# Kernel tuning notes

Measured on AMD Instinct MI355X. Metric: run time of the kernel, lower is better.

The kernel has to match this reference:

```python
import jax, jax.numpy as jnp
import numpy as np

C_Z = 128
N_HEADS = 4
HEAD_DIM = 32
TOTAL = N_HEADS * HEAD_DIM
B, N = 1, 256


def setup_inputs() -> dict:
    key = jax.random.key(0)
    ks = jax.random.split(key, 10)
    s = lambda k, sh: jax.random.normal(k, sh, dtype=jnp.float32) * 0.02
    return {
        "pair_representation": jax.random.normal(ks[0], (B, N, N, C_Z), dtype=jnp.float32),
        "ln_gamma": jnp.ones((C_Z,), jnp.float32),
        "ln_beta": jnp.zeros((C_Z,), jnp.float32),
        "Wq": s(ks[1], (C_Z, TOTAL)),
        "Wk": s(ks[2], (C_Z, TOTAL)),
        "Wv": s(ks[3], (C_Z, TOTAL)),
        "Wb": s(ks[4], (C_Z, N_HEADS)),
        "Wg": s(ks[5], (C_Z, TOTAL)),
        "bg": jnp.zeros((TOTAL,), jnp.float32),
        "Wo": s(ks[6], (TOTAL, C_Z)),
        "bo": jnp.zeros((C_Z,), jnp.float32),
    }


def reference(pair_representation, ln_gamma, ln_beta, Wq, Wk, Wv, Wb, Wg, bg, Wo, bo):
    x = pair_representation
    # LayerNorm over c_z
    mu = jnp.mean(x, axis=-1, keepdims=True)
    var = jnp.mean((x - mu) ** 2, axis=-1, keepdims=True)
    x = (x - mu) * jax.lax.rsqrt(var + 1e-5) * ln_gamma + ln_beta

    b, n, _, _ = x.shape
    split = lambda t: t.reshape(b, n, n, N_HEADS, HEAD_DIM)
    Q = split(x @ Wq)  # [b,i,j,h,d]
    K = split(x @ Wk)
    V = split(x @ Wv)
    G = jax.nn.sigmoid(split(x @ Wg + bg))
    Bias = x @ Wb  # [b,j,k,h]

    scores = jnp.einsum("bijhd,bikhd->bijkh", Q, K) / np.float32(np.sqrt(HEAD_DIM))
    scores = scores + Bias[:, None]  # broadcast over i
    attn = jax.nn.softmax(scores, axis=3)  # over k
    vals = jnp.einsum("bijkh,bikhd->bijhd", attn, V)
    vals = (G * vals).reshape(b, n, n, TOTAL)
    return vals @ Wo + bo
```

## Files before the change

### kernel.cpp

```cpp
#include <hip/hip_runtime.h>
#include <hip/hip_bf16.h>


#define QSCALE 0.17677669529663687f

typedef __attribute__((ext_vector_type(8))) short bf16x8;
typedef __attribute__((ext_vector_type(4))) float f32x4;

__device__ __forceinline__ ushort f2bf(float f) {
    uint32_t u = __builtin_bit_cast(uint32_t, f);
    uint32_t r = (u + 0x7FFFu + ((u >> 16) & 1u)) >> 16;
    return (ushort)r;
}
__device__ __forceinline__ float bf2f(ushort b) {
    return __builtin_bit_cast(float, ((uint32_t)b) << 16);
}
__device__ __forceinline__ uint pk2(float a, float b) {
    union { __hip_bfloat162 h; uint u; } cv;
    cv.h = __float22bfloat162_rn(make_float2(a, b));
    return cv.u;
}
__device__ __forceinline__ float4 ld4f(const float* p) { return *(const float4*)p; }

__global__ __launch_bounds__(256) void prep_kernel(
    const float* __restrict__ Wq, const float* __restrict__ Wk, const float* __restrict__ Wv,
    const float* __restrict__ Wb, const float* __restrict__ Wg, const float* __restrict__ Wo,
    ushort* __restrict__ Wfrag, ushort* __restrict__ WoFrag)
{
    int idx = blockIdx.x * 256 + threadIdx.x;
    if (idx < 67584) {
        int j = idx & 7, lane = (idx >> 3) & 63, ks = (idx >> 9) & 3, ct = idx >> 11;
        int n = ct * 16 + (lane & 15);
        int k = ks * 32 + (lane >> 4) * 8 + j;
        float v = 0.f;
        if (n < 128)      v = Wq[k * 128 + n] * QSCALE;
        else if (n < 256) v = Wk[k * 128 + (n - 128)];
        else if (n < 384) v = Wv[k * 128 + (n - 256)];
        else if (n < 512) v = Wg[k * 128 + (n - 384)];
        else if (n < 516) v = Wb[k * 4 + (n - 512)];
        Wfrag[idx] = f2bf(v);
    } else {
        int idx2 = idx - 67584;
        int j = idx2 & 7, lane = (idx2 >> 3) & 63, ks = (idx2 >> 9) & 3, ct = idx2 >> 11;
        int n = ct * 16 + (lane & 15);
        int k = ks * 32 + (lane >> 4) * 8 + j;
        WoFrag[idx2] = f2bf(Wo[k * 128 + n]);
    }
}

__global__ __launch_bounds__(256) void proj_kernel(
    const float* __restrict__ x, const float* __restrict__ gamma, const float* __restrict__ beta,
    const ushort* __restrict__ Wfrag, const float* __restrict__ bg,
    ushort* __restrict__ Qg, ushort* __restrict__ Kg, ushort* __restrict__ Vtg,
    ushort* __restrict__ Gg, float* __restrict__ BbF)
{
    __shared__ ushort Bs[11 * 2048];
    const int t = threadIdx.x;
    const int wave = t >> 6, lane = t & 63, m = lane & 15, quad = lane >> 4;
    const int p0 = blockIdx.x * 64;
    const int arow = p0 + wave * 16 + m;

    float4 xa[4][2];
    float sum = 0.f, ssq = 0.f;
#pragma unroll
    for (int ks = 0; ks < 4; ++ks) {
        const float* rp = x + arow * 128 + ks * 32 + quad * 8;
        xa[ks][0] = ld4f(rp);
        xa[ks][1] = ld4f(rp + 4);
#pragma unroll
        for (int q4 = 0; q4 < 2; ++q4) {
            float4 v = xa[ks][q4];
            sum += v.x + v.y + v.z + v.w;
            ssq += v.x * v.x + v.y * v.y + v.z * v.z + v.w * v.w;
        }
    }
    sum += __shfl_xor(sum, 16); ssq += __shfl_xor(ssq, 16);
    sum += __shfl_xor(sum, 32); ssq += __shfl_xor(ssq, 32);
    const float mu   = sum * (1.f / 128.f);
    const float var  = ssq * (1.f / 128.f) - mu * mu;
    const float rstd = rsqrtf(var + 1e-5f);

    bf16x8 xf[4];
#pragma unroll
    for (int ks = 0; ks < 4; ++ks) {
        union { bf16x8 v; uint u[4]; } xu;
#pragma unroll
        for (int q4 = 0; q4 < 2; ++q4) {
            const int c = ks * 32 + quad * 8 + q4 * 4;
            float4 g4 = ld4f(gamma + c);
            float4 b4 = ld4f(beta + c);
            float4 v = xa[ks][q4];
            float n0 = (v.x - mu) * rstd * g4.x + b4.x;
            float n1 = (v.y - mu) * rstd * g4.y + b4.y;
            float n2 = (v.z - mu) * rstd * g4.z + b4.z;
            float n3 = (v.w - mu) * rstd * g4.w + b4.w;
            xu.u[q4 * 2]     = pk2(n0, n1);
            xu.u[q4 * 2 + 1] = pk2(n2, n3);
        }
        xf[ks] = xu.v;
    }

    const int p = arow;
    const int i = p >> 8, j2 = p & 255;

    for (int phase = 0; phase < 3; ++phase) {
        const int ctbase = phase * 11;
        __syncthreads();
        const uint4* src = (const uint4*)(Wfrag + ctbase * 2048);
        uint4* dst = (uint4*)Bs;
#pragma unroll
        for (int r = 0; r < 11; ++r) dst[r * 256 + t] = src[r * 256 + t];
        __syncthreads();

        for (int ctl = 0; ctl < 11; ++ctl) {
            const int ct = ctbase + ctl;
            f32x4 acc = (f32x4){0.f, 0.f, 0.f, 0.f};
#pragma unroll
            for (int ks = 0; ks < 4; ++ks) {
                bf16x8 wfr = ((const bf16x8*)Bs)[(ctl * 4 + ks) * 64 + lane];
                acc = __builtin_amdgcn_mfma_f32_16x16x32_bf16(wfr, xf[ks], acc, 0, 0, 0);
            }
            if (ct < 32) {
                const int cls = ct >> 3;
                const int npb = (ct & 7) * 16 + quad * 4;
                const int hh = npb >> 5, d0 = npb & 31;
                if (cls == 2) {
                    const int vb = ((i * 4 + hh) * 32 + d0) * 256 + j2;
#pragma unroll
                    for (int r = 0; r < 4; ++r)
                        Vtg[vb + r * 256] = f2bf(acc[r]);
                } else {
                    const int off = ((i * 4 + hh) * 256 + j2) * 32 + d0;
                    uint2 u;
                    if (cls == 3) {
                        float4 bg4 = ld4f(&bg[npb]);
                        float z0 = 1.f / (1.f + __expf(-(acc[0] + bg4.x)));
                        float z1 = 1.f / (1.f + __expf(-(acc[1] + bg4.y)));
                        float z2 = 1.f / (1.f + __expf(-(acc[2] + bg4.z)));
                        float z3 = 1.f / (1.f + __expf(-(acc[3] + bg4.w)));
                        u.x = pk2(z0, z1); u.y = pk2(z2, z3);
                        *(uint2*)(&Gg[off]) = u;
                    } else {
                        u.x = pk2(acc[0], acc[1]); u.y = pk2(acc[2], acc[3]);
                        if (cls == 0) *(uint2*)(&Qg[off]) = u;
                        else          *(uint2*)(&Kg[off]) = u;
                    }
                }
            } else if (quad == 0) {
#pragma unroll
                for (int r = 0; r < 4; ++r) {
                    int addr = (((r * 16 + (i >> 4)) * 16 + (j2 >> 4)) * 64 +
                                ((j2 & 15) >> 2) * 16 + (i & 15)) * 4 + (j2 & 3);
                    BbF[addr] = acc[r];
                }
            }
        }
    }
}

__global__ __launch_bounds__(256) void attn_kernel(
    const ushort* __restrict__ Qg, const ushort* __restrict__ Kg, const ushort* __restrict__ Vtg,
    const ushort* __restrict__ Gg, const float* __restrict__ BbF, ushort* __restrict__ gvals)
{
    __shared__ ushort Pl[4][64 * 72];
    const int t = threadIdx.x;
    const int wave = t >> 6, lane = t & 63, m = lane & 15, quad = lane >> 4;
    const int ih = blockIdx.x, i = ih >> 2, h = ih & 3;

    const int j0 = wave * 64;
    bf16x8 qf[4];
#pragma unroll
    for (int jt = 0; jt < 4; ++jt)
        qf[jt] = *(const bf16x8*)(Qg + ih * 8192 + (j0 + jt * 16 + m) * 32 + quad * 8);

    f32x4 O[4][2];
    float lsum[4];
#pragma unroll
    for (int jt = 0; jt < 4; ++jt) {
        O[jt][0] = (f32x4){0.f, 0.f, 0.f, 0.f};
        O[jt][1] = (f32x4){0.f, 0.f, 0.f, 0.f};
        lsum[jt] = 0.f;
    }

    for (int kt2 = 0; kt2 < 4; ++kt2) {
        const int k0 = kt2 * 64;
        bf16x8 kf[4];
#pragma unroll
        for (int kk = 0; kk < 4; ++kk)
            kf[kk] = *(const bf16x8*)(Kg + ih * 8192 + (k0 + kk * 16 + m) * 32 + quad * 8);

#pragma unroll
        for (int jt = 0; jt < 4; ++jt) {
            const int jtg = wave * 4 + jt;
#pragma unroll
            for (int kk = 0; kk < 4; ++kk) {
                const int ktg = kt2 * 4 + kk;
                f32x4 bias = *(const f32x4*)(BbF + (((h * 16 + jtg) * 16 + ktg) * 64 + lane) * 4);
                f32x4 S = __builtin_amdgcn_mfma_f32_16x16x32_bf16(kf[kk], qf[jt], bias, 0, 0, 0);
                float pv0 = __expf(S[0]);
                float pv1 = __expf(S[1]);
                float pv2 = __expf(S[2]);
                float pv3 = __expf(S[3]);
                lsum[jt] += pv0 + pv1 + pv2 + pv3;
                uint2 u; u.x = pk2(pv0, pv1); u.y = pk2(pv2, pv3);
                *(uint2*)(&Pl[wave][(jt * 16 + m) * 72 + kk * 16 + quad * 4]) = u;
            }
        }
#pragma unroll
        for (int kc = 0; kc < 2; ++kc) {
            bf16x8 pf[4], vf[2];
#pragma unroll
            for (int jt = 0; jt < 4; ++jt)
                pf[jt] = *(const bf16x8*)(&Pl[wave][(jt * 16 + m) * 72 + kc * 32 + quad * 8]);
#pragma unroll
            for (int dt = 0; dt < 2; ++dt)
                vf[dt] = *(const bf16x8*)(Vtg + (ih * 32 + dt * 16 + m) * 256 + k0 + kc * 32 + quad * 8);
#pragma unroll
            for (int jt = 0; jt < 4; ++jt)
#pragma unroll
                for (int dt = 0; dt < 2; ++dt)
                    O[jt][dt] = __builtin_amdgcn_mfma_f32_16x16x32_bf16(
                        vf[dt], pf[jt], O[jt][dt], 0, 0, 0);
        }
    }

#pragma unroll
    for (int jt = 0; jt < 4; ++jt) {
        float s = lsum[jt];
        s += __shfl_xor(s, 16);
        s += __shfl_xor(s, 32);
        lsum[jt] = 1.f / s;
    }

#pragma unroll
    for (int jt = 0; jt < 4; ++jt) {
        const int j = j0 + jt * 16 + m;
        const float rl = lsum[jt];
#pragma unroll
        for (int dt = 0; dt < 2; ++dt) {
            const int d0 = dt * 16 + quad * 4;
            ushort4 gv = *(const ushort4*)(&Gg[ih * 8192 + j * 32 + d0]);
            float v0 = O[jt][dt][0] * rl * bf2f(gv.x);
            float v1 = O[jt][dt][1] * rl * bf2f(gv.y);
            float v2 = O[jt][dt][2] * rl * bf2f(gv.z);
            float v3 = O[jt][dt][3] * rl * bf2f(gv.w);
            uint2 u; u.x = pk2(v0, v1); u.y = pk2(v2, v3);
            *(uint2*)(&gvals[(i * 256 + j) * 128 + h * 32 + d0]) = u;
        }
    }
}

__global__ __launch_bounds__(256) void oproj_kernel(
    const ushort* __restrict__ gvals, const ushort* __restrict__ WoFrag,
    const float* __restrict__ bo, float* __restrict__ out)
{
    __shared__ ushort Bs[8 * 2048];
    const int t = threadIdx.x;
    const int wave = t >> 6, lane = t & 63, m = lane & 15, quad = lane >> 4;
    const int p0 = blockIdx.x * 64;
    {
        const uint4* src = (const uint4*)WoFrag;
        uint4* dst = (uint4*)Bs;
#pragma unroll
        for (int r = 0; r < 8; ++r) dst[r * 256 + t] = src[r * 256 + t];
    }
    bf16x8 gf[4];
    const int p = p0 + wave * 16 + m;
#pragma unroll
    for (int ks = 0; ks < 4; ++ks)
        gf[ks] = *(const bf16x8*)(gvals + p * 128 + ks * 32 + quad * 8);
    __syncthreads();

#pragma unroll
    for (int ct = 0; ct < 8; ++ct) {
        f32x4 acc = (f32x4){0.f, 0.f, 0.f, 0.f};
#pragma unroll
        for (int ks = 0; ks < 4; ++ks) {
            bf16x8 wfr = ((const bf16x8*)Bs)[(ct * 4 + ks) * 64 + lane];
            acc = __builtin_amdgcn_mfma_f32_16x16x32_bf16(wfr, gf[ks], acc, 0, 0, 0);
        }
        const int c0 = ct * 16 + quad * 4;
        float4 bov = ld4f(&bo[c0]);
        float4 v = make_float4(acc[0] + bov.x, acc[1] + bov.y,
                               acc[2] + bov.z, acc[3] + bov.w);
        *(float4*)(&out[p * 128 + c0]) = v;
    }
}

extern "C" void kernel_launch(void* const* d_in, const int* in_sizes, int n_in,
                              void* d_out, int out_size, void* d_ws, size_t ws_size,
                              hipStream_t stream) {
    const float* x     = (const float*)d_in[0];
    const float* gamma = (const float*)d_in[1];
    const float* beta  = (const float*)d_in[2];
    const float* Wq    = (const float*)d_in[3];
    const float* Wk    = (const float*)d_in[4];
    const float* Wv    = (const float*)d_in[5];
    const float* Wb    = (const float*)d_in[6];
    const float* Wg    = (const float*)d_in[7];
    const float* bg    = (const float*)d_in[8];
    const float* Wo    = (const float*)d_in[9];
    const float* bo    = (const float*)d_in[10];

    ushort* ws     = (ushort*)d_ws;
    ushort* Wfrag  = ws;
    ushort* WoFrag = Wfrag + 67584;
    ushort* Qg     = WoFrag + 16384;
    ushort* Kg     = Qg + 8388608;
    ushort* Vtg    = Kg + 8388608;
    ushort* Gg     = Vtg + 8388608;
    ushort* gvals  = Gg + 8388608;
    float*  BbF    = (float*)(gvals + 8388608);

    prep_kernel<<<328, 256, 0, stream>>>(Wq, Wk, Wv, Wb, Wg, Wo, Wfrag, WoFrag);
    proj_kernel<<<1024, 256, 0, stream>>>(x, gamma, beta, Wfrag, bg, Qg, Kg, Vtg, Gg, BbF);
    attn_kernel<<<1024, 256, 0, stream>>>(Qg, Kg, Vtg, Gg, BbF, gvals);
    oproj_kernel<<<1024, 256, 0, stream>>>(gvals, WoFrag, bo, (float*)d_out);
}
```

Baseline: 173.4 us.

## Fuse projection, attention and output projection into one per-row kernel

Replaces the separate projection, attention and output-projection kernels with a single fused kernel per row i. It keeps K, V, Q and the gated values in 160KB of LDS with XOR swizzling, which removes the global round-trips of the Q/K/V/gvals intermediates. The pair bias moves to its own LayerNorm+matvec kernel so it is ready before the fused pass. The cost is only 256 blocks of 512 threads with heavy LDS use, so occupancy is low and the gate values still pass through global memory.

```diff
diff --git a/kernel.cpp b/kernel.cpp
--- a/kernel.cpp
+++ b/kernel.cpp
@@ -20,27 +20,25 @@
     cv.h = __float22bfloat162_rn(make_float2(a, b));
     return cv.u;
 }
-__device__ __forceinline__ float4 ld4f(const float* p) { return *(const float4*)p; }
 
 __global__ __launch_bounds__(256) void prep_kernel(
     const float* __restrict__ Wq, const float* __restrict__ Wk, const float* __restrict__ Wv,
-    const float* __restrict__ Wb, const float* __restrict__ Wg, const float* __restrict__ Wo,
+    const float* __restrict__ Wg, const float* __restrict__ Wo,
     ushort* __restrict__ Wfrag, ushort* __restrict__ WoFrag)
 {
     int idx = blockIdx.x * 256 + threadIdx.x;
-    if (idx < 67584) {
+    if (idx < 65536) {
         int j = idx & 7, lane = (idx >> 3) & 63, ks = (idx >> 9) & 3, ct = idx >> 11;
         int n = ct * 16 + (lane & 15);
         int k = ks * 32 + (lane >> 4) * 8 + j;
-        float v = 0.f;
+        float v;
         if (n < 128)      v = Wq[k * 128 + n] * QSCALE;
         else if (n < 256) v = Wk[k * 128 + (n - 128)];
         else if (n < 384) v = Wv[k * 128 + (n - 256)];
-        else if (n < 512) v = Wg[k * 128 + (n - 384)];
-        else if (n < 516) v = Wb[k * 4 + (n - 512)];
+        else              v = Wg[k * 128 + (n - 384)];
         Wfrag[idx] = f2bf(v);
     } else {
-        int idx2 = idx - 67584;
+        int idx2 = idx - 65536;
         int j = idx2 & 7, lane = (idx2 >> 3) & 63, ks = (idx2 >> 9) & 3, ct = idx2 >> 11;
         int n = ct * 16 + (lane & 15);
         int k = ks * 32 + (lane >> 4) * 8 + j;
@@ -48,242 +46,371 @@
     }
 }
 
-__global__ __launch_bounds__(256) void proj_kernel(
+__global__ __launch_bounds__(256) void bias_kernel(
     const float* __restrict__ x, const float* __restrict__ gamma, const float* __restrict__ beta,
-    const ushort* __restrict__ Wfrag, const float* __restrict__ bg,
-    ushort* __restrict__ Qg, ushort* __restrict__ Kg, ushort* __restrict__ Vtg,
-    ushort* __restrict__ Gg, float* __restrict__ BbF)
+    const float* __restrict__ Wb, float* __restrict__ BbF)
 {
-    __shared__ ushort Bs[11 * 2048];
+    __shared__ float WbS[512];
+    __shared__ float gS[128];
+    __shared__ float bS[128];
     const int t = threadIdx.x;
+    if (t < 128)      { *(f32x4*)&WbS[t * 4] = *(const f32x4*)(Wb + t * 4); }
+    else if (t < 160) { int c = (t - 128) * 4; *(f32x4*)&gS[c] = *(const f32x4*)(gamma + c); }
+    else if (t < 192) { int c = (t - 160) * 4; *(f32x4*)&bS[c] = *(const f32x4*)(beta + c); }
+    __syncthreads();
+
     const int wave = t >> 6, lane = t & 63, m = lane & 15, quad = lane >> 4;
-    const int p0 = blockIdx.x * 64;
-    const int arow = p0 + wave * 16 + m;
-
-    float4 xa[4][2];
+    const int p = blockIdx.x * 64 + wave * 16 + m;
+
+    const float* rp0 = x + (size_t)p * 128;
+    f32x4 xa[4][2];
     float sum = 0.f, ssq = 0.f;
 #pragma unroll
     for (int ks = 0; ks < 4; ++ks) {
-        const float* rp = x + arow * 128 + ks * 32 + quad * 8;
-        xa[ks][0] = ld4f(rp);
-        xa[ks][1] = ld4f(rp + 4);
+        xa[ks][0] = *(const f32x4*)(rp0 + ks * 32 + quad * 8);
+        xa[ks][1] = *(const f32x4*)(rp0 + ks * 32 + quad * 8 + 4);
 #pragma unroll
         for (int q4 = 0; q4 < 2; ++q4) {
-            float4 v = xa[ks][q4];
-            sum += v.x + v.y + v.z + v.w;
-            ssq += v.x * v.x + v.y * v.y + v.z * v.z + v.w * v.w;
+            f32x4 v = xa[ks][q4];
+            sum += v[0] + v[1] + v[2] + v[3];
+            ssq += v[0]*v[0] + v[1]*v[1] + v[2]*v[2] + v[3]*v[3];
         }
     }
     sum += __shfl_xor(sum, 16); ssq += __shfl_xor(ssq, 16);
     sum += __shfl_xor(sum, 32); ssq += __shfl_xor(ssq, 32);
     const float mu   = sum * (1.f / 128.f);
-    const float var  = ssq * (1.f / 128.f) - mu * mu;
-    const float rstd = rsqrtf(var + 1e-5f);
-
-    bf16x8 xf[4];
+    const float rstd = rsqrtf(ssq * (1.f / 128.f) - mu * mu + 1e-5f);
+
+    float b0 = 0.f, b1 = 0.f, b2 = 0.f, b3 = 0.f;
 #pragma unroll
     for (int ks = 0; ks < 4; ++ks) {
-        union { bf16x8 v; uint u[4]; } xu;
 #pragma unroll
         for (int q4 = 0; q4 < 2; ++q4) {
             const int c = ks * 32 + quad * 8 + q4 * 4;
-            float4 g4 = ld4f(gamma + c);
-            float4 b4 = ld4f(beta + c);
-            float4 v = xa[ks][q4];
-            float n0 = (v.x - mu) * rstd * g4.x + b4.x;
-            float n1 = (v.y - mu) * rstd * g4.y + b4.y;
-            float n2 = (v.z - mu) * rstd * g4.z + b4.z;
-            float n3 = (v.w - mu) * rstd * g4.w + b4.w;
-            xu.u[q4 * 2]     = pk2(n0, n1);
-            xu.u[q4 * 2 + 1] = pk2(n2, n3);
-        }
-        xf[ks] = xu.v;
-    }
-
-    const int p = arow;
-    const int i = p >> 8, j2 = p & 255;
-
-    for (int phase = 0; phase < 3; ++phase) {
-        const int ctbase = phase * 11;
-        __syncthreads();
-        const uint4* src = (const uint4*)(Wfrag + ctbase * 2048);
-        uint4* dst = (uint4*)Bs;
-#pragma unroll
-        for (int r = 0; r < 11; ++r) dst[r * 256 + t] = src[r * 256 + t];
-        __syncthreads();
-
-        for (int ctl = 0; ctl < 11; ++ctl) {
-            const int ct = ctbase + ctl;
-            f32x4 acc = (f32x4){0.f, 0.f, 0.f, 0.f};
-#pragma unroll
-            for (int ks = 0; ks < 4; ++ks) {
-                bf16x8 wfr = ((const bf16x8*)Bs)[(ctl * 4 + ks) * 64 + lane];
-                acc = __builtin_amdgcn_mfma_f32_16x16x32_bf16(wfr, xf[ks], acc, 0, 0, 0);
-            }
-            if (ct < 32) {
-                const int cls = ct >> 3;
-                const int npb = (ct & 7) * 16 + quad * 4;
-                const int hh = npb >> 5, d0 = npb & 31;
-                if (cls == 2) {
-                    const int vb = ((i * 4 + hh) * 32 + d0) * 256 + j2;
-#pragma unroll
-                    for (int r = 0; r < 4; ++r)
-                        Vtg[vb + r * 256] = f2bf(acc[r]);
-                } else {
-                    const int off = ((i * 4 + hh) * 256 + j2) * 32 + d0;
-                    uint2 u;
-                    if (cls == 3) {
-                        float4 bg4 = ld4f(&bg[npb]);
-                        float z0 = 1.f / (1.f + __expf(-(acc[0] + bg4.x)));
-                        float z1 = 1.f / (1.f + __expf(-(acc[1] + bg4.y)));
-                        float z2 = 1.f / (1.f + __expf(-(acc[2] + bg4.z)));
-                        float z3 = 1.f / (1.f + __expf(-(acc[3] + bg4.w)));
-                        u.x = pk2(z0, z1); u.y = pk2(z2, z3);
-                        *(uint2*)(&Gg[off]) = u;
-                    } else {
-                        u.x = pk2(acc[0], acc[1]); u.y = pk2(acc[2], acc[3]);
-                        if (cls == 0) *(uint2*)(&Qg[off]) = u;
-                        else          *(uint2*)(&Kg[off]) = u;
-                    }
-                }
-            } else if (quad == 0) {
-#pragma unroll
-                for (int r = 0; r < 4; ++r) {
-                    int addr = (((r * 16 + (i >> 4)) * 16 + (j2 >> 4)) * 64 +
-                                ((j2 & 15) >> 2) * 16 + (i & 15)) * 4 + (j2 & 3);
-                    BbF[addr] = acc[r];
-                }
-            }
-        }
-    }
-}
-
-__global__ __launch_bounds__(256) void attn_kernel(
-    const ushort* __restrict__ Qg, const ushort* __restrict__ Kg, const ushort* __restrict__ Vtg,
-    const ushort* __restrict__ Gg, const float* __restrict__ BbF, ushort* __restrict__ gvals)
+            f32x4 v = xa[ks][q4];
+#pragma unroll
+            for (int e = 0; e < 4; ++e) {
+                float xn = (v[e] - mu) * rstd * gS[c + e] + bS[c + e];
+                f32x4 w = *(const f32x4*)&WbS[(c + e) * 4];
+                b0 += xn * w[0]; b1 += xn * w[1]; b2 += xn * w[2]; b3 += xn * w[3];
+            }
+        }
+    }
+    b0 += __shfl_xor(b0, 16); b1 += __shfl_xor(b1, 16); b2 += __shfl_xor(b2, 16); b3 += __shfl_xor(b3, 16);
+    b0 += __shfl_xor(b0, 32); b1 += __shfl_xor(b1, 32); b2 += __shfl_xor(b2, 32); b3 += __shfl_xor(b3, 32);
+
+    if (quad == 0) {
+        const int row = p >> 8, col = p & 255;
+        float bb[4] = {b0, b1, b2, b3};
+#pragma unroll
+        for (int r = 0; r < 4; ++r) {
+            int addr = (((r * 16 + (row >> 4)) * 16 + (col >> 4)) * 64 +
+                        ((col & 15) >> 2) * 16 + (row & 15)) * 4 + (col & 3);
+            BbF[addr] = bb[r];
+        }
+    }
+}
+
+__device__ __forceinline__ void stage32(ushort* dst, const ushort* src, int t) {
+    const uint4* s = (const uint4*)src;
+    uint4* d = (uint4*)dst;
+#pragma unroll
+    for (int c = 0; c < 4; ++c) d[c * 512 + t] = s[c * 512 + t];
+}
+
+__global__ __launch_bounds__(512, 2) void fused_kernel(
+    const float* __restrict__ x, const float* __restrict__ gamma, const float* __restrict__ beta,
+    const ushort* __restrict__ Wfrag, const ushort* __restrict__ WoFrag,
+    const float* __restrict__ bg, const float* __restrict__ bo,
+    const float* __restrict__ BbF, ushort* __restrict__ Gg, float* __restrict__ out)
 {
-    __shared__ ushort Pl[4][64 * 72];
+    extern __shared__ __align__(16) ushort smem[];
+    ushort* KL  = smem;
+    ushort* VL  = smem + 32768;
+    ushort* SCR = smem + 65536;
+
     const int t = threadIdx.x;
     const int wave = t >> 6, lane = t & 63, m = lane & 15, quad = lane >> 4;
-    const int ih = blockIdx.x, i = ih >> 2, h = ih & 3;
-
-    const int j0 = wave * 64;
-    bf16x8 qf[4];
-#pragma unroll
-    for (int jt = 0; jt < 4; ++jt)
-        qf[jt] = *(const bf16x8*)(Qg + ih * 8192 + (j0 + jt * 16 + m) * 32 + quad * 8);
-
-    f32x4 O[4][2];
-    float lsum[4];
-#pragma unroll
-    for (int jt = 0; jt < 4; ++jt) {
-        O[jt][0] = (f32x4){0.f, 0.f, 0.f, 0.f};
-        O[jt][1] = (f32x4){0.f, 0.f, 0.f, 0.f};
-        lsum[jt] = 0.f;
-    }
-
-    for (int kt2 = 0; kt2 < 4; ++kt2) {
-        const int k0 = kt2 * 64;
-        bf16x8 kf[4];
-#pragma unroll
-        for (int kk = 0; kk < 4; ++kk)
-            kf[kk] = *(const bf16x8*)(Kg + ih * 8192 + (k0 + kk * 16 + m) * 32 + quad * 8);
-
+    const int i = blockIdx.x;
+
+    bf16x8 xf[2][4];
+#pragma unroll
+    for (int grp = 0; grp < 2; ++grp) {
+        const int j = wave * 32 + grp * 16 + m;
+        const float* rp0 = x + (size_t)(i * 256 + j) * 128;
+        f32x4 xa[4][2];
+        float sum = 0.f, ssq = 0.f;
+#pragma unroll
+        for (int ks = 0; ks < 4; ++ks) {
+            xa[ks][0] = *(const f32x4*)(rp0 + ks * 32 + quad * 8);
+            xa[ks][1] = *(const f32x4*)(rp0 + ks * 32 + quad * 8 + 4);
+#pragma unroll
+            for (int q4 = 0; q4 < 2; ++q4) {
+                f32x4 v = xa[ks][q4];
+                sum += v[0] + v[1] + v[2] + v[3];
+                ssq += v[0]*v[0] + v[1]*v[1] + v[2]*v[2] + v[3]*v[3];
+            }
+        }
+        sum += __shfl_xor(sum, 16); ssq += __shfl_xor(ssq, 16);
+        sum += __shfl_xor(sum, 32); ssq += __shfl_xor(ssq, 32);
+        const float mu   = sum * (1.f / 128.f);
+        const float rstd = rsqrtf(ssq * (1.f / 128.f) - mu * mu + 1e-5f);
+#pragma unroll
+        for (int ks = 0; ks < 4; ++ks) {
+            union { bf16x8 v; uint u[4]; } xu;
+#pragma unroll
+            for (int q4 = 0; q4 < 2; ++q4) {
+                const int c = ks * 32 + quad * 8 + q4 * 4;
+                f32x4 g4 = *(const f32x4*)(gamma + c);
+                f32x4 b4 = *(const f32x4*)(beta + c);
+                f32x4 v = xa[ks][q4];
+                float n0 = (v[0] - mu) * rstd * g4[0] + b4[0];
+                float n1 = (v[1] - mu) * rstd * g4[1] + b4[1];
+                float n2 = (v[2] - mu) * rstd * g4[2] + b4[2];
+                float n3 = (v[3] - mu) * rstd * g4[3] + b4[3];
+                xu.u[q4 * 2]     = pk2(n0, n1);
+                xu.u[q4 * 2 + 1] = pk2(n2, n3);
+            }
+            xf[grp][ks] = xu.v;
+        }
+    }
+
+    stage32(SCR, Wfrag, t);
+    __syncthreads();
+#pragma unroll
+    for (int ct = 0; ct < 8; ++ct) {
+        bf16x8 wfr[4];
+#pragma unroll
+        for (int ks = 0; ks < 4; ++ks) wfr[ks] = ((const bf16x8*)SCR)[(ct * 4 + ks) * 64 + lane];
+#pragma unroll
+        for (int grp = 0; grp < 2; ++grp) {
+            f32x4 acc = (f32x4){0.f, 0.f, 0.f, 0.f};
+#pragma unroll
+            for (int ks = 0; ks < 4; ++ks)
+                acc = __builtin_amdgcn_mfma_f32_16x16x32_bf16(wfr[ks], xf[grp][ks], acc, 0, 0, 0);
+            const int pj = wave * 32 + grp * 16 + m;
+            const int c0 = ct * 16 + quad * 4;
+            const int idx = (pj * 128 + c0) ^ ((pj & 7) << 3);
+            uint2 u; u.x = pk2(acc[0], acc[1]); u.y = pk2(acc[2], acc[3]);
+            *(uint2*)(KL + idx) = u;
+        }
+    }
+    __syncthreads();
+
+    const int h = wave >> 1;
+    const int jb = (wave & 1) * 128;
+    bf16x8 qf[8];
+#pragma unroll
+    for (int jt8 = 0; jt8 < 8; ++jt8) {
+        const int j = jb + jt8 * 16 + m;
+        const int idx = (j * 128 + h * 32 + quad * 8) ^ ((j & 7) << 3);
+        qf[jt8] = *(const bf16x8*)(KL + idx);
+    }
+
+    stage32(SCR, Wfrag + 16384, t);
+    __syncthreads();
+#pragma unroll
+    for (int ct = 0; ct < 8; ++ct) {
+        bf16x8 wfr[4];
+#pragma unroll
+        for (int ks = 0; ks < 4; ++ks) wfr[ks] = ((const bf16x8*)SCR)[(ct * 4 + ks) * 64 + lane];
+        const int hk = ct >> 1;
+        const int d0 = (ct & 1) * 16 + quad * 4;
+#pragma unroll
+        for (int grp = 0; grp < 2; ++grp) {
+            f32x4 acc = (f32x4){0.f, 0.f, 0.f, 0.f};
+#pragma unroll
+            for (int ks = 0; ks < 4; ++ks)
+                acc = __builtin_amdgcn_mfma_f32_16x16x32_bf16(wfr[ks], xf[grp][ks], acc, 0, 0, 0);
+            const int k = wave * 32 + grp * 16 + m;
+            const int idx = (hk * 8192 + (k >> 1) * 64 + (k & 1) * 32 + d0) ^ (((k >> 1) & 7) << 3);
+            uint2 u; u.x = pk2(acc[0], acc[1]); u.y = pk2(acc[2], acc[3]);
+            *(uint2*)(KL + idx) = u;
+        }
+    }
+
+    __syncthreads();
+    stage32(SCR, Wfrag + 32768, t);
+    __syncthreads();
+#pragma unroll
+    for (int ct = 0; ct < 8; ++ct) {
+        bf16x8 wfr[4];
+#pragma unroll
+        for (int ks = 0; ks < 4; ++ks) wfr[ks] = ((const bf16x8*)SCR)[(ct * 4 + ks) * 64 + lane];
+        const int hv = ct >> 1;
+        const int d0 = (ct & 1) * 16 + quad * 4;
+#pragma unroll
+        for (int grp = 0; grp < 2; ++grp) {
+            f32x4 acc = (f32x4){0.f, 0.f, 0.f, 0.f};
+#pragma unroll
+            for (int ks = 0; ks < 4; ++ks)
+                acc = __builtin_amdgcn_mfma_f32_16x16x32_bf16(wfr[ks], xf[grp][ks], acc, 0, 0, 0);
+            const int k = wave * 32 + grp * 16 + m;
+#pragma unroll
+            for (int r = 0; r < 4; ++r) {
+                const int d = d0 + r;
+                const int idx = ((hv * 32 + d) * 256 + k) ^ ((d & 7) << 3);
+                VL[idx] = f2bf(acc[r]);
+            }
+        }
+    }
+
+    __syncthreads();
+    stage32(SCR, Wfrag + 49152, t);
+    __syncthreads();
+#pragma unroll
+    for (int ct = 0; ct < 8; ++ct) {
+        bf16x8 wfr[4];
+#pragma unroll
+        for (int ks = 0; ks < 4; ++ks) wfr[ks] = ((const bf16x8*)SCR)[(ct * 4 + ks) * 64 + lane];
+        const int c0 = ct * 16 + quad * 4;
+        f32x4 bg4 = *(const f32x4*)(bg + c0);
+#pragma unroll
+        for (int grp = 0; grp < 2; ++grp) {
+            f32x4 acc = (f32x4){0.f, 0.f, 0.f, 0.f};
+#pragma unroll
+            for (int ks = 0; ks < 4; ++ks)
+                acc = __builtin_amdgcn_mfma_f32_16x16x32_bf16(wfr[ks], xf[grp][ks], acc, 0, 0, 0);
+            float z0 = 1.f / (1.f + __expf(-(acc[0] + bg4[0])));
+            float z1 = 1.f / (1.f + __expf(-(acc[1] + bg4[1])));
+            float z2 = 1.f / (1.f + __expf(-(acc[2] + bg4[2])));
+            float z3 = 1.f / (1.f + __expf(-(acc[3] + bg4[3])));
+            uint2 u; u.x = pk2(z0, z1); u.y = pk2(z2, z3);
+            const int gidx = (((wave * 8 + ct) * 2 + grp) * 64 + lane) * 4;
+            *(uint2*)(Gg + (size_t)i * 32768 + gidx) = u;
+        }
+    }
+    __syncthreads();
+
+    ushort* Pw = SCR + wave * 2048;
+    f32x4 O[2][4][2];
+    float lsum[2][4];
+#pragma unroll
+    for (int u = 0; u < 2; ++u)
 #pragma unroll
         for (int jt = 0; jt < 4; ++jt) {
-            const int jtg = wave * 4 + jt;
-#pragma unroll
-            for (int kk = 0; kk < 4; ++kk) {
-                const int ktg = kt2 * 4 + kk;
-                f32x4 bias = *(const f32x4*)(BbF + (((h * 16 + jtg) * 16 + ktg) * 64 + lane) * 4);
-                f32x4 S = __builtin_amdgcn_mfma_f32_16x16x32_bf16(kf[kk], qf[jt], bias, 0, 0, 0);
-                float pv0 = __expf(S[0]);
-                float pv1 = __expf(S[1]);
-                float pv2 = __expf(S[2]);
-                float pv3 = __expf(S[3]);
-                lsum[jt] += pv0 + pv1 + pv2 + pv3;
-                uint2 u; u.x = pk2(pv0, pv1); u.y = pk2(pv2, pv3);
-                *(uint2*)(&Pl[wave][(jt * 16 + m) * 72 + kk * 16 + quad * 4]) = u;
-            }
-        }
-#pragma unroll
-        for (int kc = 0; kc < 2; ++kc) {
-            bf16x8 pf[4], vf[2];
+            O[u][jt][0] = (f32x4){0.f, 0.f, 0.f, 0.f};
+            O[u][jt][1] = (f32x4){0.f, 0.f, 0.f, 0.f};
+            lsum[u][jt] = 0.f;
+        }
+
+#pragma unroll
+    for (int u = 0; u < 2; ++u) {
+        const int jq = (wave & 1) * 2 + u;
+        for (int kh = 0; kh < 8; ++kh) {
+            const int k0 = kh * 32;
+            bf16x8 kf[2];
+#pragma unroll
+            for (int kk = 0; kk < 2; ++kk) {
+                const int k = k0 + kk * 16 + m;
+                const int idx = (h * 8192 + (k >> 1) * 64 + (k & 1) * 32 + quad * 8) ^ (((k >> 1) & 7) << 3);
+                kf[kk] = *(const bf16x8*)(KL + idx);
+            }
+#pragma unroll
+            for (int jt = 0; jt < 4; ++jt) {
+                const int jtg = jq * 4 + jt;
+#pragma unroll
+                for (int kk = 0; kk < 2; ++kk) {
+                    const int ktg = kh * 2 + kk;
+                    f32x4 S = *(const f32x4*)(BbF + (((h * 16 + jtg) * 16 + ktg) * 64 + lane) * 4);
+                    S = __builtin_amdgcn_mfma_f32_16x16x32_bf16(kf[kk], qf[u * 4 + jt], S, 0, 0, 0);
+                    float p0 = __expf(S[0]), p1 = __expf(S[1]);
+                    float p2 = __expf(S[2]), p3 = __expf(S[3]);
+                    lsum[u][jt] += p0 + p1 + p2 + p3;
+                    const int jl = jt * 16 + m;
+                    const int pidx = ((jl >> 1) * 64 + (jl & 1) * 32 + kk * 16 + quad * 4) ^ (((jl >> 1) & 7) << 3);
+                    uint2 up; up.x = pk2(p0, p1); up.y = pk2(p2, p3);
+                    *(uint2*)(Pw + pidx) = up;
+                }
+            }
+            bf16x8 vf[2], pf[4];
+#pragma unroll
+            for (int dt = 0; dt < 2; ++dt) {
+                const int d = dt * 16 + m;
+                const int idx = ((h * 32 + d) * 256 + k0 + quad * 8) ^ ((d & 7) << 3);
+                vf[dt] = *(const bf16x8*)(VL + idx);
+            }
+#pragma unroll
+            for (int jt = 0; jt < 4; ++jt) {
+                const int jl = jt * 16 + m;
+                const int pidx = ((jl >> 1) * 64 + (jl & 1) * 32 + quad * 8) ^ (((jl >> 1) & 7) << 3);
+                pf[jt] = *(const bf16x8*)(Pw + pidx);
+            }
 #pragma unroll
             for (int jt = 0; jt < 4; ++jt)
-                pf[jt] = *(const bf16x8*)(&Pl[wave][(jt * 16 + m) * 72 + kc * 32 + quad * 8]);
-#pragma unroll
-            for (int dt = 0; dt < 2; ++dt)
-                vf[dt] = *(const bf16x8*)(Vtg + (ih * 32 + dt * 16 + m) * 256 + k0 + kc * 32 + quad * 8);
-#pragma unroll
-            for (int jt = 0; jt < 4; ++jt)
 #pragma unroll
                 for (int dt = 0; dt < 2; ++dt)
-                    O[jt][dt] = __builtin_amdgcn_mfma_f32_16x16x32_bf16(
-                        vf[dt], pf[jt], O[jt][dt], 0, 0, 0);
-        }
-    }
-
-#pragma unroll
-    for (int jt = 0; jt < 4; ++jt) {
-        float s = lsum[jt];
-        s += __shfl_xor(s, 16);
-        s += __shfl_xor(s, 32);
-        lsum[jt] = 1.f / s;
-    }
-
-#pragma unroll
-    for (int jt = 0; jt < 4; ++jt) {
-        const int j = j0 + jt * 16 + m;
-        const float rl = lsum[jt];
-#pragma unroll
-        for (int dt = 0; dt < 2; ++dt) {
-            const int d0 = dt * 16 + quad * 4;
-            ushort4 gv = *(const ushort4*)(&Gg[ih * 8192 + j * 32 + d0]);
-            float v0 = O[jt][dt][0] * rl * bf2f(gv.x);
-            float v1 = O[jt][dt][1] * rl * bf2f(gv.y);
-            float v2 = O[jt][dt][2] * rl * bf2f(gv.z);
-            float v3 = O[jt][dt][3] * rl * bf2f(gv.w);
-            uint2 u; u.x = pk2(v0, v1); u.y = pk2(v2, v3);
-            *(uint2*)(&gvals[(i * 256 + j) * 128 + h * 32 + d0]) = u;
-        }
-    }
-}
-
-__global__ __launch_bounds__(256) void oproj_kernel(
-    const ushort* __restrict__ gvals, const ushort* __restrict__ WoFrag,
-    const float* __restrict__ bo, float* __restrict__ out)
-{
-    __shared__ ushort Bs[8 * 2048];
-    const int t = threadIdx.x;
-    const int wave = t >> 6, lane = t & 63, m = lane & 15, quad = lane >> 4;
-    const int p0 = blockIdx.x * 64;
-    {
-        const uint4* src = (const uint4*)WoFrag;
-        uint4* dst = (uint4*)Bs;
-#pragma unroll
-        for (int r = 0; r < 8; ++r) dst[r * 256 + t] = src[r * 256 + t];
-    }
-    bf16x8 gf[4];
-    const int p = p0 + wave * 16 + m;
-#pragma unroll
-    for (int ks = 0; ks < 4; ++ks)
-        gf[ks] = *(const bf16x8*)(gvals + p * 128 + ks * 32 + quad * 8);
-    __syncthreads();
-
+                    O[u][jt][dt] = __builtin_amdgcn_mfma_f32_16x16x32_bf16(
+                        vf[dt], pf[jt], O[u][jt][dt], 0, 0, 0);
+        }
+    }
+
+#pragma unroll
+    for (int u = 0; u < 2; ++u)
+#pragma unroll
+        for (int jt = 0; jt < 4; ++jt) {
+            float s = lsum[u][jt];
+            s += __shfl_xor(s, 16);
+            s += __shfl_xor(s, 32);
+            lsum[u][jt] = 1.f / s;
+        }
+
+    __syncthreads();
+
+#pragma unroll
+    for (int u = 0; u < 2; ++u) {
+        const int jq = (wave & 1) * 2 + u;
+#pragma unroll
+        for (int jt = 0; jt < 4; ++jt) {
+            const int j = jq * 64 + jt * 16 + m;
+            const float rl = lsum[u][jt];
+#pragma unroll
+            for (int dt = 0; dt < 2; ++dt) {
+                const int c0 = h * 32 + dt * 16 + quad * 4;
+                const int gaddr = ((((j >> 5) * 8 + (h * 2 + dt)) * 2 + ((j >> 4) & 1)) * 64 + quad * 16 + m) * 4;
+                ushort4 gv = *(const ushort4*)(Gg + (size_t)i * 32768 + gaddr);
+                float v0 = O[u][jt][dt][0] * rl * bf2f(gv.x);
+                float v1 = O[u][jt][dt][1] * rl * bf2f(gv.y);
+                float v2 = O[u][jt][dt][2] * rl * bf2f(gv.z);
+                float v3 = O[u][jt][dt][3] * rl * bf2f(gv.w);
+                const int idx = (j * 128 + c0) ^ ((j & 7) << 3);
+                uint2 uo; uo.x = pk2(v0, v1); uo.y = pk2(v2, v3);
+                *(uint2*)(KL + idx) = uo;
+            }
+        }
+    }
+
+    stage32(SCR, WoFrag, t);
+    __syncthreads();
+
+    bf16x8 gf[2][4];
+#pragma unroll
+    for (int grp = 0; grp < 2; ++grp) {
+        const int pl = wave * 32 + grp * 16 + m;
+#pragma unroll
+        for (int ks = 0; ks < 4; ++ks) {
+            const int idx = (pl * 128 + ks * 32 + quad * 8) ^ ((pl & 7) << 3);
+            gf[grp][ks] = *(const bf16x8*)(KL + idx);
+        }
+    }
 #pragma unroll
     for (int ct = 0; ct < 8; ++ct) {
-        f32x4 acc = (f32x4){0.f, 0.f, 0.f, 0.f};
-#pragma unroll
-        for (int ks = 0; ks < 4; ++ks) {
-            bf16x8 wfr = ((const bf16x8*)Bs)[(ct * 4 + ks) * 64 + lane];
-            acc = __builtin_amdgcn_mfma_f32_16x16x32_bf16(wfr, gf[ks], acc, 0, 0, 0);
-        }
+        bf16x8 wfr[4];
+#pragma unroll
+        for (int ks = 0; ks < 4; ++ks) wfr[ks] = ((const bf16x8*)SCR)[(ct * 4 + ks) * 64 + lane];
         const int c0 = ct * 16 + quad * 4;
-        float4 bov = ld4f(&bo[c0]);
-        float4 v = make_float4(acc[0] + bov.x, acc[1] + bov.y,
-                               acc[2] + bov.z, acc[3] + bov.w);
-        *(float4*)(&out[p * 128 + c0]) = v;
+        f32x4 bov = *(const f32x4*)(bo + c0);
+#pragma unroll
+        for (int grp = 0; grp < 2; ++grp) {
+            f32x4 acc = (f32x4){0.f, 0.f, 0.f, 0.f};
+#pragma unroll
+            for (int ks = 0; ks < 4; ++ks)
+                acc = __builtin_amdgcn_mfma_f32_16x16x32_bf16(wfr[ks], gf[grp][ks], acc, 0, 0, 0);
+            const int p = i * 256 + wave * 32 + grp * 16 + m;
+            float4 vout = make_float4(acc[0] + bov[0], acc[1] + bov[1],
+                                      acc[2] + bov[2], acc[3] + bov[3]);
+            *(float4*)(out + (size_t)p * 128 + c0) = vout;
+        }
     }
 }
 
@@ -302,18 +429,21 @@
     const float* Wo    = (const float*)d_in[9];
     const float* bo    = (const float*)d_in[10];
 
-    ushort* ws     = (ushort*)d_ws;
-    ushort* Wfrag  = ws;
-    ushort* WoFrag = Wfrag + 67584;
-    ushort* Qg     = WoFrag + 16384;
-    ushort* Kg     = Qg + 8388608;
-    ushort* Vtg    = Kg + 8388608;
-    ushort* Gg     = Vtg + 8388608;
-    ushort* gvals  = Gg + 8388608;
-    float*  BbF    = (float*)(gvals + 8388608);
-
-    prep_kernel<<<328, 256, 0, stream>>>(Wq, Wk, Wv, Wb, Wg, Wo, Wfrag, WoFrag);
-    proj_kernel<<<1024, 256, 0, stream>>>(x, gamma, beta, Wfrag, bg, Qg, Kg, Vtg, Gg, BbF);
-    attn_kernel<<<1024, 256, 0, stream>>>(Qg, Kg, Vtg, Gg, BbF, gvals);
-    oproj_kernel<<<1024, 256, 0, stream>>>(gvals, WoFrag, bo, (float*)d_out);
-}
+    ushort* ws      = (ushort*)d_ws;
+    ushort* Wfrag   = ws;
+    ushort* WoFragp = ws + 65536;
+    ushort* Gg      = ws + 81920;
+    float*  BbF     = (float*)(ws + 81920 + 8388608);
+
+    static bool attr_set = false;
+    if (!attr_set) {
+        hipFuncSetAttribute((const void*)fused_kernel,
+                            hipFuncAttributeMaxDynamicSharedMemorySize, 163840);
+        attr_set = true;
+    }
+
+    prep_kernel<<<320, 256, 0, stream>>>(Wq, Wk, Wv, Wg, Wo, Wfrag, WoFragp);
+    bias_kernel<<<1024, 256, 0, stream>>>(x, gamma, beta, Wb, BbF);
+    fused_kernel<<<256, 512, 163840, stream>>>(x, gamma, beta, Wfrag, WoFragp,
+                                               bg, bo, BbF, Gg, (float*)d_out);
+}
```

After: 148.2 us. -14.6%, faster.
